# Optimization experiments

Measured on AMD Instinct MI355X. Metric: run time of the kernel, lower is better.

## Reference

```python
import jax, jax.numpy as jnp
import numpy as np

LMAX = 5
L = LMAX + 1            # L_out = L_in = 6
DIM = L * L             # 36 spherical-harmonic coefficients
RES_B = 2 * L           # 12 beta points (Gauss-Legendre in cos(beta))
RES_A = 2 * L           # 12 alpha points (uniform)
CORRELATION = 3
REPEATS = np.arange(1, 2 * L, 2)  # [1,3,5,7,9,11]: ir.dim per l, mul=1 in irreps_out


def _normalized_assoc_legendre(lmax, x):
    """Fully (L2 on sphere) normalized associated Legendre Pbar_l^m(x), no CS phase.
    Returns dict[(l,m)] -> np.ndarray over x."""
    P = {}
    s = np.sqrt(np.maximum(1.0 - x * x, 0.0))
    P[(0, 0)] = np.full_like(x, np.sqrt(1.0 / (4.0 * np.pi)))
    for m in range(1, lmax + 1):
        P[(m, m)] = np.sqrt((2.0 * m + 1.0) / (2.0 * m)) * s * P[(m - 1, m - 1)]
    for m in range(0, lmax):
        P[(m + 1, m)] = np.sqrt(2.0 * m + 3.0) * x * P[(m, m)]
    for m in range(0, lmax + 1):
        for l in range(m + 2, lmax + 1):
            a = np.sqrt((4.0 * l * l - 1.0) / (l * l - m * m))
            b = np.sqrt(((l - 1.0) ** 2 - m * m) / (4.0 * (l - 1.0) ** 2 - 1.0))
            P[(l, m)] = a * (x * P[(l - 1, m)] - b * P[(l - 2, m)])
    return P


def build_s2grid(lmax, res_beta, res_alpha):
    """Y: [res_beta, res_alpha, (lmax+1)^2] real orthonormal SH samples.
    Yw: Y with quadrature weights so that einsum(f, Yw) inverts einsum(c, Y)."""
    xq, wq = np.polynomial.legendre.leggauss(res_beta)  # nodes in cos(beta)
    alpha = np.arange(res_alpha) * (2.0 * np.pi / res_alpha)
    P = _normalized_assoc_legendre(lmax, xq)
    dim = (lmax + 1) ** 2
    Y = np.zeros((res_beta, res_alpha, dim))
    sqrt2 = np.sqrt(2.0)
    for l in range(lmax + 1):
        for m in range(-l, l + 1):
            idx = l * l + l + m
            plm = P[(l, abs(m))]
            if m > 0:
                ang = sqrt2 * np.cos(m * alpha)
            elif m == 0:
                ang = np.ones(res_alpha)
            else:
                ang = sqrt2 * np.sin(-m * alpha)
            Y[:, :, idx] = plm[:, None] * ang[None, :]
    Yw = Y * wq[:, None, None] * (2.0 * np.pi / res_alpha)
    return jnp.asarray(Y, jnp.float32), jnp.asarray(Yw, jnp.float32)


def setup_inputs() -> dict:
    key = jax.random.key(0)
    k1, k2, k3 = jax.random.split(key, 3)
    atom_feat = jax.random.normal(k1, (4096, 128, DIM), dtype=jnp.float32)
    atom_type = jax.random.uniform(k2, (4096, 10), dtype=jnp.float32)
    weights = jax.random.normal(k3, (CORRELATION, 10, 128, L), dtype=jnp.float32)
    return {"atom_feat": atom_feat, "atom_type": atom_type, "weights": weights}


def reference(atom_feat, atom_type, weights):
    Y, Yw = build_s2grid(LMAX, RES_B, RES_A)

    def to_grid(c):      # [n, C, DIM] -> [n, C, beta, alpha]
        return jnp.einsum('nck,bak->ncba', c, Y)

    def from_grid(f):    # [n, C, beta, alpha] -> [n, C, DIM]
        return jnp.einsum('ncba,bak->nck', f, Yw)

    def apply_w(w):      # w: [E, C, L]; atom-type-weighted, expanded to DIM
        wn = jnp.einsum('ne,ecl->ncl', atom_type, w)  # [n, C, L]
        return jnp.repeat(wn, REPEATS, axis=-1, total_repeat_length=DIM)

    feat_grid = to_grid(atom_feat)  # reused across correlation orders
    prod = atom_feat
    result = apply_w(weights[0]) * prod
    for nu in range(1, CORRELATION):
        # Gaunt tensor product via S2 grid: pointwise multiply on the sphere
        prod = from_grid(to_grid(prod) * feat_grid)
        result = result + apply_w(weights[nu]) * prod
    return jnp.squeeze(result)
```

## Files before the change

kernel.cpp:

```cpp
#include <hip/hip_runtime.h>
#include <stdint.h>

namespace ct {

constexpr double PI_ = 3.14159265358979323846;

constexpr double csqrt(double x) {
  double g = x > 1.0 ? x : 1.0;
  for (int i = 0; i < 40; ++i) g = 0.5 * (g + x / g);
  return g;
}
constexpr double ccos(double x) {
  double x2 = x * x, t = 1.0, s = 1.0;
  for (int k = 1; k <= 16; ++k) { t *= -x2 / ((2.0 * k - 1.0) * (2.0 * k)); s += t; }
  return s;
}
constexpr double csin(double x) {
  double x2 = x * x, t = x, s = x;
  for (int k = 1; k <= 16; ++k) { t *= -x2 / ((2.0 * k) * (2.0 * k + 1.0)); s += t; }
  return s;
}

struct GL { double x[12]; double w[12]; };

constexpr GL gl12() {
  GL g{};
  for (int i = 0; i < 12; ++i) {
    double x = ccos(PI_ * (i + 0.75) / 12.5);
    for (int it = 0; it < 50; ++it) {
      double p0 = 1.0, p1 = x;
      for (int k = 2; k <= 12; ++k) { double pk = ((2.0 * k - 1.0) * x * p1 - (k - 1.0) * p0) / k; p0 = p1; p1 = pk; }
      double dp = 12.0 * (x * p1 - p0) / (x * x - 1.0);
      x -= p1 / dp;
    }
    double p0 = 1.0, p1 = x;
    for (int k = 2; k <= 12; ++k) { double pk = ((2.0 * k - 1.0) * x * p1 - (k - 1.0) * p0) / k; p0 = p1; p1 = pk; }
    double dp = 12.0 * (x * p1 - p0) / (x * x - 1.0);
    g.x[i] = x;
    g.w[i] = 2.0 / ((1.0 - x * x) * dp * dp);
  }
  return g;
}

struct Tab {
  double PA[12][36];
  double PB[12][36];
  double ANG[12][36];
};

constexpr Tab make_tab() {
  Tab t{};
  GL g = gl12();
  for (int b = 0; b < 12; ++b) {
    double x = g.x[b];
    double s = csqrt(1.0 - x * x);
    double P[6][6] = {};
    P[0][0] = csqrt(1.0 / (4.0 * PI_));
    for (int m = 1; m <= 5; ++m) P[m][m] = csqrt((2.0 * m + 1.0) / (2.0 * m)) * s * P[m - 1][m - 1];
    for (int m = 0; m < 5; ++m)  P[m + 1][m] = csqrt(2.0 * m + 3.0) * x * P[m][m];
    for (int m = 0; m <= 5; ++m)
      for (int l = m + 2; l <= 5; ++l) {
        double aa = csqrt((4.0 * l * l - 1.0) / (double)(l * l - m * m));
        double bb = csqrt(((l - 1.0) * (l - 1.0) - (double)(m * m)) / (4.0 * (l - 1.0) * (l - 1.0) - 1.0));
        P[l][m] = aa * (x * P[l - 1][m] - bb * P[l - 2][m]);
      }
    for (int l = 0; l <= 5; ++l)
      for (int m = -l; m <= l; ++m) {
        int k = l * l + l + m, am = m < 0 ? -m : m;
        t.PA[b][k] = P[l][am];
        t.PB[b][k] = P[l][am] * g.w[b] * (2.0 * PI_ / 12.0);
      }
  }
  double r2 = csqrt(2.0);
  for (int a = 0; a < 12; ++a)
    for (int l = 0; l <= 5; ++l)
      for (int m = -l; m <= l; ++m) {
        int k = l * l + l + m, am = m < 0 ? -m : m;
        double v = 1.0;
        if (m != 0) {
          int qq = (am * a) % 12;
          double ang = 2.0 * PI_ * qq / 12.0;
          if (ang > PI_) ang -= 2.0 * PI_;
          v = (m > 0) ? r2 * ccos(ang) : r2 * csin(ang);
        }
        t.ANG[a][k] = v;
      }
  return t;
}

constexpr Tab TD = make_tab();

constexpr unsigned f2bf(double x) {
  if (x == 0.0) return 0u;
  unsigned s = 0u; double a = x;
  if (a < 0.0) { s = 0x8000u; a = -a; }
  int e = 127;
  while (a >= 2.0) { a *= 0.5; ++e; }
  while (a < 1.0)  { a *= 2.0; --e; }
  double md = (a - 1.0) * 128.0;
  int mi = (int)md;
  double fr = md - mi;
  if (fr > 0.5 || (fr == 0.5 && (mi & 1))) ++mi;
  if (mi == 128) { mi = 0; ++e; }
  return s | ((unsigned)e << 7) | (unsigned)mi;
}

constexpr double syn_val(int k, int n) {
  if (k >= 36 || n >= 144) return 0.0;
  int b = n / 12, a = n % 12;
  return TD.PA[b][k] * TD.ANG[a][k];
}
constexpr double ana_val(int kp, int np) {
  if (kp >= 144 || np >= 36) return 0.0;
  int b = kp / 12, a = kp % 12;
  return TD.PB[b][np] * TD.ANG[a][np];
}

struct alignas(16) Syn32 { unsigned v[3 * 5 * 64 * 4]; };
struct alignas(16) Ana32 { unsigned v[9 * 2 * 64 * 4]; };

constexpr Syn32 make_syn32() {
  Syn32 F{};
  for (int ks = 0; ks < 3; ++ks)
    for (int nt = 0; nt < 5; ++nt)
      for (int lane = 0; lane < 64; ++lane)
        for (int jp = 0; jp < 4; ++jp) {
          int h = lane >> 5, n = nt * 32 + (lane & 31);
          int k0 = ks * 16 + h * 8 + jp * 2;
          F.v[((ks * 5 + nt) * 64 + lane) * 4 + jp] =
              f2bf(syn_val(k0, n)) | (f2bf(syn_val(k0 + 1, n)) << 16);
        }
  return F;
}
constexpr Ana32 make_ana32() {
  Ana32 F{};
  for (int ks = 0; ks < 9; ++ks)
    for (int nt = 0; nt < 2; ++nt)
      for (int lane = 0; lane < 64; ++lane)
        for (int jp = 0; jp < 4; ++jp) {
          int h = lane >> 5, n = nt * 32 + (lane & 31);
          int k0 = ks * 16 + h * 8 + jp * 2;
          F.v[((ks * 2 + nt) * 64 + lane) * 4 + jp] =
              f2bf(ana_val(k0, n)) | (f2bf(ana_val(k0 + 1, n)) << 16);
        }
  return F;
}

}

__device__ constexpr ct::Syn32 SYNB = ct::make_syn32();
__device__ constexpr ct::Ana32 ANAB = ct::make_ana32();

typedef __attribute__((ext_vector_type(8))) short short8;
typedef __attribute__((ext_vector_type(16))) float f32x16;

union S8 { short8 s; unsigned u[4]; uint2 u2[2]; };

__device__ __forceinline__ unsigned short bfr(float x) {
  return (unsigned short)((__float_as_uint(x) + 0x8000u) >> 16);
}
__device__ __forceinline__ unsigned pk2(float x, float y) {
  return (unsigned)bfr(x) | ((unsigned)bfr(y) << 16);
}
__device__ __forceinline__ float lo16(unsigned u) { return __uint_as_float(u << 16); }
__device__ __forceinline__ float hi16(unsigned u) { return __uint_as_float(u & 0xFFFF0000u); }

__device__ __forceinline__ short8 synf(int ks, int nt, int lane) {
  const uint4* p = reinterpret_cast<const uint4*>(SYNB.v) + (ks * 5 + nt) * 64 + lane;
  uint4 t = *p; S8 r; r.u[0] = t.x; r.u[1] = t.y; r.u[2] = t.z; r.u[3] = t.w; return r.s;
}
__device__ __forceinline__ short8 anaf(int ks, int nt, int lane) {
  const uint4* p = reinterpret_cast<const uint4*>(ANAB.v) + (ks * 2 + nt) * 64 + lane;
  uint4 t = *p; S8 r; r.u[0] = t.x; r.u[1] = t.y; r.u[2] = t.z; r.u[3] = t.w; return r.s;
}

#define FWS 148
#define COS 52

__global__ __launch_bounds__(128, 2)
void gaunt32_kernel(const float* __restrict__ feat,
                    const float* __restrict__ atype,
                    const float* __restrict__ wts,
                    float* __restrict__ out) {
  __shared__ unsigned short FW[2][32 * FWS];
  __shared__ unsigned short CO[2][32 * COS];
  __shared__ float WN[2][18 * 32];

  const int tid = threadIdx.x;
  const int ws = __builtin_amdgcn_readfirstlane(tid >> 6);
  const int lane = tid & 63;
  const int m = lane & 31, h = lane >> 5;
  const int mtile = blockIdx.x * 2 + ws;
  const int rowbase = mtile * 32;
  const int atom = mtile >> 2;
  const int chb = (mtile & 3) * 32;

  unsigned short* fw = FW[ws];
  unsigned short* co = CO[ws];
  float* wn = WN[ws];

  const float* fr = feat + (rowbase + m) * 36;
  S8 af[3];
  {
    float4 a = *reinterpret_cast<const float4*>(fr + h * 8);
    float4 b = *reinterpret_cast<const float4*>(fr + h * 8 + 4);
    af[0].u[0] = pk2(a.x, a.y); af[0].u[1] = pk2(a.z, a.w);
    af[0].u[2] = pk2(b.x, b.y); af[0].u[3] = pk2(b.z, b.w);
    a = *reinterpret_cast<const float4*>(fr + 16 + h * 8);
    b = *reinterpret_cast<const float4*>(fr + 20 + h * 8);
    af[1].u[0] = pk2(a.x, a.y); af[1].u[1] = pk2(a.z, a.w);
    af[1].u[2] = pk2(b.x, b.y); af[1].u[3] = pk2(b.z, b.w);
    af[2].u[0] = 0; af[2].u[1] = 0; af[2].u[2] = 0; af[2].u[3] = 0;
    if (h == 0) {
      a = *reinterpret_cast<const float4*>(fr + 32);
      af[2].u[0] = pk2(a.x, a.y); af[2].u[1] = pk2(a.z, a.w);
    }
  }

  unsigned fpk[5][8];
#pragma unroll
  for (int nt = 0; nt < 5; ++nt) {
    f32x16 acc = {0.f, 0.f, 0.f, 0.f, 0.f, 0.f, 0.f, 0.f,
                  0.f, 0.f, 0.f, 0.f, 0.f, 0.f, 0.f, 0.f};
#pragma unroll
    for (int ks = 0; ks < 3; ++ks)
      acc = __builtin_amdgcn_mfma_f32_32x32x16_bf16(af[ks].s, synf(ks, nt, lane), acc, 0, 0, 0);
    const int col = nt * 32 + m;
#pragma unroll
    for (int g = 0; g < 4; ++g) {
      fpk[nt][2 * g + 0] = pk2(acc[4 * g + 0], acc[4 * g + 1]);
      fpk[nt][2 * g + 1] = pk2(acc[4 * g + 2], acc[4 * g + 3]);
    }
    if (col < 144) {
#pragma unroll
      for (int g = 0; g < 4; ++g)
#pragma unroll
        for (int i = 0; i < 4; ++i) {
          float v = acc[4 * g + i];
          fw[(i + 8 * g + 4 * h) * FWS + col] = bfr(v * v);
        }
    }
  }

  S8 ga[9];
  {
    const unsigned short* fr2 = &fw[m * FWS + h * 8];
#pragma unroll
    for (int ks = 0; ks < 9; ++ks) {
      ga[ks].u2[0] = *reinterpret_cast<const uint2*>(fr2 + ks * 16);
      ga[ks].u2[1] = *reinterpret_cast<const uint2*>(fr2 + ks * 16 + 4);
    }
  }
  f32x16 p1[2];
#pragma unroll
  for (int nt = 0; nt < 2; ++nt) {
    f32x16 acc = {0.f, 0.f, 0.f, 0.f, 0.f, 0.f, 0.f, 0.f,
                  0.f, 0.f, 0.f, 0.f, 0.f, 0.f, 0.f, 0.f};
#pragma unroll
    for (int ks = 0; ks < 9; ++ks)
      acc = __builtin_amdgcn_mfma_f32_32x32x16_bf16(ga[ks].s, anaf(ks, nt, lane), acc, 0, 0, 0);
    p1[nt] = acc;
  }

#pragma unroll
  for (int nt = 0; nt < 2; ++nt) {
    const int col = nt * 32 + m;
    if (col < 48) {
#pragma unroll
      for (int g = 0; g < 4; ++g)
#pragma unroll
        for (int i = 0; i < 4; ++i)
          co[(i + 8 * g + 4 * h) * COS + col] = bfr(p1[nt][4 * g + i]);
    }
  }

  S8 ca[3];
  {
    const unsigned short* cr = &co[m * COS + h * 8];
#pragma unroll
    for (int ks = 0; ks < 3; ++ks) {
      ca[ks].u2[0] = *reinterpret_cast<const uint2*>(cr + ks * 16);
      ca[ks].u2[1] = *reinterpret_cast<const uint2*>(cr + ks * 16 + 4);
    }
  }
#pragma unroll
  for (int nt = 0; nt < 5; ++nt) {
    f32x16 acc = {0.f, 0.f, 0.f, 0.f, 0.f, 0.f, 0.f, 0.f,
                  0.f, 0.f, 0.f, 0.f, 0.f, 0.f, 0.f, 0.f};
#pragma unroll
    for (int ks = 0; ks < 3; ++ks)
      acc = __builtin_amdgcn_mfma_f32_32x32x16_bf16(ca[ks].s, synf(ks, nt, lane), acc, 0, 0, 0);
    const int col = nt * 32 + m;
    if (col < 144) {
#pragma unroll
      for (int g = 0; g < 4; ++g)
#pragma unroll
        for (int i = 0; i < 4; ++i) {
          unsigned pk = fpk[nt][2 * g + (i >> 1)];
          float f = (i & 1) ? hi16(pk) : lo16(pk);
          fw[(i + 8 * g + 4 * h) * FWS + col] = bfr(acc[4 * g + i] * f);
        }
    }
  }

  {
    const unsigned short* fr2 = &fw[m * FWS + h * 8];
#pragma unroll
    for (int ks = 0; ks < 9; ++ks) {
      ga[ks].u2[0] = *reinterpret_cast<const uint2*>(fr2 + ks * 16);
      ga[ks].u2[1] = *reinterpret_cast<const uint2*>(fr2 + ks * 16 + 4);
    }
  }
  f32x16 p2[2];
#pragma unroll
  for (int nt = 0; nt < 2; ++nt) {
    f32x16 acc = {0.f, 0.f, 0.f, 0.f, 0.f, 0.f, 0.f, 0.f,
                  0.f, 0.f, 0.f, 0.f, 0.f, 0.f, 0.f, 0.f};
#pragma unroll
    for (int ks = 0; ks < 9; ++ks)
      acc = __builtin_amdgcn_mfma_f32_32x32x16_bf16(ga[ks].s, anaf(ks, nt, lane), acc, 0, 0, 0);
    p2[nt] = acc;
  }

  {
    float at[10];
#pragma unroll
    for (int e = 0; e < 10; ++e) at[e] = atype[atom * 10 + e];
#pragma unroll
    for (int t = 0; t < 9; ++t) {
      const int p = h + 2 * t;
      const int nu = p >= 12 ? 2 : (p >= 6 ? 1 : 0);
      const int l = p - nu * 6;
      const float* wb = wts + ((nu * 10) * 128 + chb + m) * 6 + l;
      float s = 0.f;
#pragma unroll
      for (int e = 0; e < 10; ++e) s += at[e] * wb[e * 768];
      wn[p * 32 + m] = s;
    }
  }

#pragma unroll
  for (int nt = 0; nt < 2; ++nt) {
    const int col = nt * 32 + m;
    if (col < 36) {
      const int lc = col >= 25 ? 5 : col >= 16 ? 4 : col >= 9 ? 3 : col >= 4 ? 2 : col >= 1 ? 1 : 0;
#pragma unroll
      for (int g = 0; g < 4; ++g)
#pragma unroll
        for (int i = 0; i < 4; ++i) {
          const int row = i + 8 * g + 4 * h;
          const float c0 = feat[(rowbase + row) * 36 + col];
          const float w0 = wn[(lc + 0) * 32 + row];
          const float w1 = wn[(lc + 6) * 32 + row];
          const float w2 = wn[(lc + 12) * 32 + row];
          out[(size_t)(rowbase + row) * 36 + col] =
              w0 * c0 + w1 * p1[nt][4 * g + i] + w2 * p2[nt][4 * g + i];
        }
    }
  }
}

extern "C" void kernel_launch(void* const* d_in, const int* in_sizes, int n_in,
                              void* d_out, int out_size, void* d_ws, size_t ws_size,
                              hipStream_t stream) {
  const float* feat = (const float*)d_in[0];
  const float* atype = (const float*)d_in[1];
  const float* wts = (const float*)d_in[2];
  float* out = (float*)d_out;
  (void)in_sizes; (void)n_in; (void)out_size; (void)d_ws; (void)ws_size;

  gaunt32_kernel<<<8192, 128, 0, stream>>>(feat, atype, wts, out);
}
```

Measured before the change: 226.6 us.

## Transpose MFMA operands and use permlane swaps to drop LDS staging

```diff
diff --git a/kernel.cpp b/kernel.cpp
--- a/kernel.cpp
+++ b/kernel.cpp
@@ -174,32 +174,34 @@
   uint4 t = *p; S8 r; r.u[0] = t.x; r.u[1] = t.y; r.u[2] = t.z; r.u[3] = t.w; return r.s;
 }
 
-#define FWS 148
-#define COS 52
-
-__global__ __launch_bounds__(128, 2)
+__device__ __forceinline__ S8 mkfrag(unsigned P0, unsigned P1, unsigned Q0, unsigned Q1) {
+  auto r0 = __builtin_amdgcn_permlane32_swap((int)P0, (int)Q0, false, false);
+  auto r1 = __builtin_amdgcn_permlane32_swap((int)P1, (int)Q1, false, false);
+  S8 f;
+  f.u[0] = (unsigned)r0[0];
+  f.u[1] = (unsigned)r1[0];
+  f.u[2] = (unsigned)r0[1];
+  f.u[3] = (unsigned)r1[1];
+  return f;
+}
+
+#define Z16 {0.f,0.f,0.f,0.f,0.f,0.f,0.f,0.f,0.f,0.f,0.f,0.f,0.f,0.f,0.f,0.f}
+
+__global__ __launch_bounds__(256, 3)
 void gaunt32_kernel(const float* __restrict__ feat,
                     const float* __restrict__ atype,
                     const float* __restrict__ wts,
                     float* __restrict__ out) {
-  __shared__ unsigned short FW[2][32 * FWS];
-  __shared__ unsigned short CO[2][32 * COS];
-  __shared__ float WN[2][18 * 32];
-
   const int tid = threadIdx.x;
   const int ws = __builtin_amdgcn_readfirstlane(tid >> 6);
   const int lane = tid & 63;
   const int m = lane & 31, h = lane >> 5;
-  const int mtile = blockIdx.x * 2 + ws;
+  const int mtile = blockIdx.x * 4 + ws;
   const int rowbase = mtile * 32;
   const int atom = mtile >> 2;
   const int chb = (mtile & 3) * 32;
 
-  unsigned short* fw = FW[ws];
-  unsigned short* co = CO[ws];
-  float* wn = WN[ws];
-
-  const float* fr = feat + (rowbase + m) * 36;
+  const float* fr = feat + (size_t)(rowbase + m) * 36;
   S8 af[3];
   {
     float4 a = *reinterpret_cast<const float4*>(fr + h * 8);
@@ -217,146 +219,121 @@
     }
   }
 
-  unsigned fpk[5][8];
-#pragma unroll
-  for (int nt = 0; nt < 5; ++nt) {
-    f32x16 acc = {0.f, 0.f, 0.f, 0.f, 0.f, 0.f, 0.f, 0.f,
-                  0.f, 0.f, 0.f, 0.f, 0.f, 0.f, 0.f, 0.f};
+  f32x16 p1[2]; p1[0] = (f32x16)Z16; p1[1] = (f32x16)Z16;
+  unsigned fpre[5][8];
+#pragma unroll
+  for (int mt = 0; mt < 5; ++mt) {
+    f32x16 a1 = Z16;
 #pragma unroll
     for (int ks = 0; ks < 3; ++ks)
-      acc = __builtin_amdgcn_mfma_f32_32x32x16_bf16(af[ks].s, synf(ks, nt, lane), acc, 0, 0, 0);
-    const int col = nt * 32 + m;
-#pragma unroll
-    for (int g = 0; g < 4; ++g) {
-      fpk[nt][2 * g + 0] = pk2(acc[4 * g + 0], acc[4 * g + 1]);
-      fpk[nt][2 * g + 1] = pk2(acc[4 * g + 2], acc[4 * g + 3]);
-    }
-    if (col < 144) {
-#pragma unroll
-      for (int g = 0; g < 4; ++g)
-#pragma unroll
-        for (int i = 0; i < 4; ++i) {
-          float v = acc[4 * g + i];
-          fw[(i + 8 * g + 4 * h) * FWS + col] = bfr(v * v);
-        }
-    }
-  }
-
-  S8 ga[9];
+      a1 = __builtin_amdgcn_mfma_f32_32x32x16_bf16(synf(ks, mt, lane), af[ks].s, a1, 0, 0, 0);
+#pragma unroll
+    for (int q = 0; q < 2; ++q) {
+      const int ksg = 2 * mt + q;
+      if (ksg < 9) {
+#pragma unroll
+        for (int t = 0; t < 4; ++t)
+          fpre[mt][4 * q + t] = pk2(a1[8 * q + 2 * t], a1[8 * q + 2 * t + 1]);
+        S8 fb = mkfrag(pk2(a1[8*q+0]*a1[8*q+0], a1[8*q+1]*a1[8*q+1]),
+                       pk2(a1[8*q+2]*a1[8*q+2], a1[8*q+3]*a1[8*q+3]),
+                       pk2(a1[8*q+4]*a1[8*q+4], a1[8*q+5]*a1[8*q+5]),
+                       pk2(a1[8*q+6]*a1[8*q+6], a1[8*q+7]*a1[8*q+7]));
+        p1[0] = __builtin_amdgcn_mfma_f32_32x32x16_bf16(anaf(ksg, 0, lane), fb.s, p1[0], 0, 0, 0);
+        p1[1] = __builtin_amdgcn_mfma_f32_32x32x16_bf16(anaf(ksg, 1, lane), fb.s, p1[1], 0, 0, 0);
+      }
+    }
+  }
+
+  S8 b3[3];
+  b3[0] = mkfrag(pk2(p1[0][0],  p1[0][1]),  pk2(p1[0][2],  p1[0][3]),
+                 pk2(p1[0][4],  p1[0][5]),  pk2(p1[0][6],  p1[0][7]));
+  b3[1] = mkfrag(pk2(p1[0][8],  p1[0][9]),  pk2(p1[0][10], p1[0][11]),
+                 pk2(p1[0][12], p1[0][13]), pk2(p1[0][14], p1[0][15]));
+  b3[2] = mkfrag(pk2(p1[1][0],  p1[1][1]),  pk2(p1[1][2],  p1[1][3]),
+                 pk2(p1[1][4],  p1[1][5]),  pk2(p1[1][6],  p1[1][7]));
+
+  f32x16 p2[2]; p2[0] = (f32x16)Z16; p2[1] = (f32x16)Z16;
+#pragma unroll
+  for (int mt = 0; mt < 5; ++mt) {
+    f32x16 a3 = Z16;
+#pragma unroll
+    for (int ks = 0; ks < 3; ++ks)
+      a3 = __builtin_amdgcn_mfma_f32_32x32x16_bf16(synf(ks, mt, lane), b3[ks].s, a3, 0, 0, 0);
+#pragma unroll
+    for (int q = 0; q < 2; ++q) {
+      const int ksg = 2 * mt + q;
+      if (ksg < 9) {
+        float g0 = a3[8*q+0] * lo16(fpre[mt][4*q+0]);
+        float g1 = a3[8*q+1] * hi16(fpre[mt][4*q+0]);
+        float g2 = a3[8*q+2] * lo16(fpre[mt][4*q+1]);
+        float g3 = a3[8*q+3] * hi16(fpre[mt][4*q+1]);
+        float g4 = a3[8*q+4] * lo16(fpre[mt][4*q+2]);
+        float g5 = a3[8*q+5] * hi16(fpre[mt][4*q+2]);
+        float g6 = a3[8*q+6] * lo16(fpre[mt][4*q+3]);
+        float g7 = a3[8*q+7] * hi16(fpre[mt][4*q+3]);
+        S8 gb = mkfrag(pk2(g0, g1), pk2(g2, g3), pk2(g4, g5), pk2(g6, g7));
+        p2[0] = __builtin_amdgcn_mfma_f32_32x32x16_bf16(anaf(ksg, 0, lane), gb.s, p2[0], 0, 0, 0);
+        p2[1] = __builtin_amdgcn_mfma_f32_32x32x16_bf16(anaf(ksg, 1, lane), gb.s, p2[1], 0, 0, 0);
+      }
+    }
+  }
+
+  float4 c4[4];
+#pragma unroll
+  for (int g = 0; g < 4; ++g)
+    c4[g] = *reinterpret_cast<const float4*>(fr + 8 * g + 4 * h);
+  float4 c5 = {0.f, 0.f, 0.f, 0.f};
+  if (h == 0) c5 = *reinterpret_cast<const float4*>(fr + 32);
+
+  float wnv[3][6];
   {
-    const unsigned short* fr2 = &fw[m * FWS + h * 8];
-#pragma unroll
-    for (int ks = 0; ks < 9; ++ks) {
-      ga[ks].u2[0] = *reinterpret_cast<const uint2*>(fr2 + ks * 16);
-      ga[ks].u2[1] = *reinterpret_cast<const uint2*>(fr2 + ks * 16 + 4);
-    }
-  }
-  f32x16 p1[2];
-#pragma unroll
-  for (int nt = 0; nt < 2; ++nt) {
-    f32x16 acc = {0.f, 0.f, 0.f, 0.f, 0.f, 0.f, 0.f, 0.f,
-                  0.f, 0.f, 0.f, 0.f, 0.f, 0.f, 0.f, 0.f};
-#pragma unroll
-    for (int ks = 0; ks < 9; ++ks)
-      acc = __builtin_amdgcn_mfma_f32_32x32x16_bf16(ga[ks].s, anaf(ks, nt, lane), acc, 0, 0, 0);
-    p1[nt] = acc;
-  }
-
-#pragma unroll
-  for (int nt = 0; nt < 2; ++nt) {
-    const int col = nt * 32 + m;
-    if (col < 48) {
-#pragma unroll
-      for (int g = 0; g < 4; ++g)
-#pragma unroll
-        for (int i = 0; i < 4; ++i)
-          co[(i + 8 * g + 4 * h) * COS + col] = bfr(p1[nt][4 * g + i]);
-    }
-  }
-
-  S8 ca[3];
-  {
-    const unsigned short* cr = &co[m * COS + h * 8];
-#pragma unroll
-    for (int ks = 0; ks < 3; ++ks) {
-      ca[ks].u2[0] = *reinterpret_cast<const uint2*>(cr + ks * 16);
-      ca[ks].u2[1] = *reinterpret_cast<const uint2*>(cr + ks * 16 + 4);
-    }
-  }
-#pragma unroll
-  for (int nt = 0; nt < 5; ++nt) {
-    f32x16 acc = {0.f, 0.f, 0.f, 0.f, 0.f, 0.f, 0.f, 0.f,
-                  0.f, 0.f, 0.f, 0.f, 0.f, 0.f, 0.f, 0.f};
-#pragma unroll
-    for (int ks = 0; ks < 3; ++ks)
-      acc = __builtin_amdgcn_mfma_f32_32x32x16_bf16(ca[ks].s, synf(ks, nt, lane), acc, 0, 0, 0);
-    const int col = nt * 32 + m;
-    if (col < 144) {
-#pragma unroll
-      for (int g = 0; g < 4; ++g)
-#pragma unroll
-        for (int i = 0; i < 4; ++i) {
-          unsigned pk = fpk[nt][2 * g + (i >> 1)];
-          float f = (i & 1) ? hi16(pk) : lo16(pk);
-          fw[(i + 8 * g + 4 * h) * FWS + col] = bfr(acc[4 * g + i] * f);
-        }
-    }
-  }
-
-  {
-    const unsigned short* fr2 = &fw[m * FWS + h * 8];
-#pragma unroll
-    for (int ks = 0; ks < 9; ++ks) {
-      ga[ks].u2[0] = *reinterpret_cast<const uint2*>(fr2 + ks * 16);
-      ga[ks].u2[1] = *reinterpret_cast<const uint2*>(fr2 + ks * 16 + 4);
-    }
-  }
-  f32x16 p2[2];
-#pragma unroll
-  for (int nt = 0; nt < 2; ++nt) {
-    f32x16 acc = {0.f, 0.f, 0.f, 0.f, 0.f, 0.f, 0.f, 0.f,
-                  0.f, 0.f, 0.f, 0.f, 0.f, 0.f, 0.f, 0.f};
-#pragma unroll
-    for (int ks = 0; ks < 9; ++ks)
-      acc = __builtin_amdgcn_mfma_f32_32x32x16_bf16(ga[ks].s, anaf(ks, nt, lane), acc, 0, 0, 0);
-    p2[nt] = acc;
-  }
-
-  {
-    float at[10];
-#pragma unroll
-    for (int e = 0; e < 10; ++e) at[e] = atype[atom * 10 + e];
-#pragma unroll
-    for (int t = 0; t < 9; ++t) {
-      const int p = h + 2 * t;
-      const int nu = p >= 12 ? 2 : (p >= 6 ? 1 : 0);
-      const int l = p - nu * 6;
-      const float* wb = wts + ((nu * 10) * 128 + chb + m) * 6 + l;
-      float s = 0.f;
-#pragma unroll
-      for (int e = 0; e < 10; ++e) s += at[e] * wb[e * 768];
-      wn[p * 32 + m] = s;
-    }
-  }
-
-#pragma unroll
-  for (int nt = 0; nt < 2; ++nt) {
-    const int col = nt * 32 + m;
-    if (col < 36) {
-      const int lc = col >= 25 ? 5 : col >= 16 ? 4 : col >= 9 ? 3 : col >= 4 ? 2 : col >= 1 ? 1 : 0;
-#pragma unroll
-      for (int g = 0; g < 4; ++g)
-#pragma unroll
-        for (int i = 0; i < 4; ++i) {
-          const int row = i + 8 * g + 4 * h;
-          const float c0 = feat[(rowbase + row) * 36 + col];
-          const float w0 = wn[(lc + 0) * 32 + row];
-          const float w1 = wn[(lc + 6) * 32 + row];
-          const float w2 = wn[(lc + 12) * 32 + row];
-          out[(size_t)(rowbase + row) * 36 + col] =
-              w0 * c0 + w1 * p1[nt][4 * g + i] + w2 * p2[nt][4 * g + i];
-        }
-    }
+    const float* ab = atype + atom * 10;
+    float at_[10];
+#pragma unroll
+    for (int e = 0; e < 10; ++e) at_[e] = ab[e];
+    const float* wb = wts + (size_t)(chb + m) * 6;
+#pragma unroll
+    for (int nu = 0; nu < 3; ++nu) {
+#pragma unroll
+      for (int l = 0; l < 6; ++l) wnv[nu][l] = 0.f;
+#pragma unroll
+      for (int e = 0; e < 10; ++e) {
+        const float* p = wb + (size_t)(nu * 10 + e) * 768;
+        float2 x = *reinterpret_cast<const float2*>(p);
+        float2 y = *reinterpret_cast<const float2*>(p + 2);
+        float2 z = *reinterpret_cast<const float2*>(p + 4);
+        wnv[nu][0] += at_[e] * x.x; wnv[nu][1] += at_[e] * x.y;
+        wnv[nu][2] += at_[e] * y.x; wnv[nu][3] += at_[e] * y.y;
+        wnv[nu][4] += at_[e] * z.x; wnv[nu][5] += at_[e] * z.y;
+      }
+    }
+  }
+
+  constexpr int LC0t[4][4] = {{0,1,1,1},{2,3,3,3},{4,4,4,4},{4,5,5,5}};
+  constexpr int LC1t[4][4] = {{2,2,2,2},{3,3,3,3},{4,4,4,4},{5,5,5,5}};
+  float* o0 = out + (size_t)(rowbase + m) * 36;
+#pragma unroll
+  for (int g = 0; g < 4; ++g) {
+    const float* cp = reinterpret_cast<const float*>(&c4[g]);
+    float ov[4];
+#pragma unroll
+    for (int i = 0; i < 4; ++i) {
+      const float w0 = h ? wnv[0][LC1t[g][i]] : wnv[0][LC0t[g][i]];
+      const float w1 = h ? wnv[1][LC1t[g][i]] : wnv[1][LC0t[g][i]];
+      const float w2 = h ? wnv[2][LC1t[g][i]] : wnv[2][LC0t[g][i]];
+      ov[i] = w0 * cp[i] + w1 * p1[0][4 * g + i] + w2 * p2[0][4 * g + i];
+    }
+    float4 o4 = {ov[0], ov[1], ov[2], ov[3]};
+    *reinterpret_cast<float4*>(o0 + 8 * g + 4 * h) = o4;
+  }
+  if (h == 0) {
+    const float* cp = reinterpret_cast<const float*>(&c5);
+    float ov[4];
+#pragma unroll
+    for (int i = 0; i < 4; ++i)
+      ov[i] = wnv[0][5] * cp[i] + wnv[1][5] * p1[1][i] + wnv[2][5] * p2[1][i];
+    float4 o4 = {ov[0], ov[1], ov[2], ov[3]};
+    *reinterpret_cast<float4*>(o0 + 32) = o4;
   }
 }
 
@@ -369,5 +346,5 @@
   float* out = (float*)d_out;
   (void)in_sizes; (void)n_in; (void)out_size; (void)d_ws; (void)ws_size;
 
-  gaunt32_kernel<<<8192, 128, 0, stream>>>(feat, atype, wts, out);
-}
+  gaunt32_kernel<<<4096, 256, 0, stream>>>(feat, atype, wts, out);
+}
```

Measured after the change: 370.5 us. 1.63x slower.
